# Kernel tuning notes

Measured on AMD Instinct MI355X. Metric: run time of the kernel, lower is better.

## Reference

```python
import jax, jax.numpy as jnp
import numpy as np

D_MODEL = 1024
N_HEADS = 16
HEAD_DIM = D_MODEL // N_HEADS
ROPE_THETA = 10000.0


def setup_inputs() -> dict:
    key = jax.random.key(0)
    ks = jax.random.split(key, 5)
    B, S = 4, 2048
    x = jax.random.normal(ks[0], (B, S, D_MODEL), dtype=jnp.float32)
    Wq = jax.random.normal(ks[1], (D_MODEL, D_MODEL), dtype=jnp.float32) * 0.02
    Wk = jax.random.normal(ks[2], (D_MODEL, D_MODEL), dtype=jnp.float32) * 0.02
    Wv = jax.random.normal(ks[3], (D_MODEL, D_MODEL), dtype=jnp.float32) * 0.02
    Wo = jax.random.normal(ks[4], (D_MODEL, D_MODEL), dtype=jnp.float32) * 0.02
    token_positions = jnp.arange(S, dtype=jnp.int32)
    return {"x": x, "token_positions": token_positions, "Wq": Wq, "Wk": Wk, "Wv": Wv, "Wo": Wo}


def apply_rope(t, positions):
    # t: [B, H, S, Dk]; positions: [S]
    half = HEAD_DIM // 2
    inv_freq = 1.0 / (ROPE_THETA ** (jnp.arange(half, dtype=jnp.float32) * 2.0 / HEAD_DIM))
    angles = positions.astype(jnp.float32)[:, None] * inv_freq[None, :]  # [S, half]
    cos = jnp.cos(angles)[None, None]  # [1,1,S,half]
    sin = jnp.sin(angles)[None, None]
    t_even = t[..., 0::2]
    t_odd = t[..., 1::2]
    rot_even = t_even * cos - t_odd * sin
    rot_odd = t_even * sin + t_odd * cos
    out = jnp.stack([rot_even, rot_odd], axis=-1)  # [B,H,S,half,2]
    return out.reshape(t.shape)


def reference(x, token_positions, Wq, Wk, Wv, Wo):
    B, S, _ = x.shape
    H, Dk = N_HEADS, HEAD_DIM
    # QKV projections, split heads -> [B, H, S, Dk]
    q = (x @ Wq).reshape(B, S, H, Dk).transpose(0, 2, 1, 3)
    k = (x @ Wk).reshape(B, S, H, Dk).transpose(0, 2, 1, 3)
    v = (x @ Wv).reshape(B, S, H, Dk).transpose(0, 2, 1, 3)
    q = apply_rope(q, token_positions)
    k = apply_rope(k, token_positions)
    scale = 1.0 / jnp.sqrt(jnp.asarray(Dk, dtype=x.dtype))
    scores = jnp.einsum('bhqd,bhkd->bhqk', q, k) * scale
    causal = jnp.tril(jnp.ones((S, S), dtype=bool))
    scores = jnp.where(causal[None, None], scores, jnp.asarray(-jnp.inf, dtype=scores.dtype))
    attn = jax.nn.softmax(scores, axis=-1)
    ctx = jnp.einsum('bhqk,bhkd->bhqd', attn, v)  # [B,H,S,Dk]
    ctx = ctx.transpose(0, 2, 1, 3).reshape(B, S, H * Dk)
    return ctx @ Wo
```

## Files before the change

kernel.cpp:

```cpp
#include <hip/hip_runtime.h>

typedef unsigned short u16;
typedef unsigned int   u32;
typedef __bf16  bf16x8 __attribute__((ext_vector_type(8)));
typedef float   f32x4  __attribute__((ext_vector_type(4)));
typedef float   f32x16 __attribute__((ext_vector_type(16)));
typedef u16     u16x4  __attribute__((ext_vector_type(4)));
typedef u16     u16x8  __attribute__((ext_vector_type(8)));
typedef u32     u32x4  __attribute__((ext_vector_type(4)));

#define D_MODEL 1024
#define N_HEADS 16
#define HEAD_DIM 64
#define BATCH 4
#define SEQ 2048
#define MROWS (BATCH*SEQ)

__device__ __forceinline__ u16 f2bf(float f){
  unsigned u = __builtin_bit_cast(unsigned, f);
  u += 0x7fffu + ((u >> 16) & 1u);
  return (u16)(u >> 16);
}
__device__ __forceinline__ float bf2f(u16 h){
  unsigned u = ((unsigned)h) << 16;
  return __builtin_bit_cast(float, u);
}
__device__ __forceinline__ u32 cvtpk(float a, float b){
  u32 r; asm("v_cvt_pk_bf16_f32 %0, %1, %2" : "=v"(r) : "v"(a), "v"(b)); return r;
}
__device__ __forceinline__ void gload_lds16(const u16* g, u16* l){
  __builtin_amdgcn_global_load_lds((const __attribute__((address_space(1))) void*)g,
                                   (__attribute__((address_space(3))) void*)l, 16, 0, 0);
}
#define MFMA16(a,b,c) __builtin_amdgcn_mfma_f32_16x16x32_bf16((a),(b),(c),0,0,0)

__global__ void k_prep(const float* __restrict__ x, const float* __restrict__ Wq,
                       const float* __restrict__ Wk, const float* __restrict__ Wv,
                       const float* __restrict__ Wo, const int* __restrict__ pos,
                       u16* __restrict__ xb, u16* __restrict__ wt, float2* __restrict__ tab){
  __shared__ float t[32][33];
  const int blk = blockIdx.x, tid = threadIdx.x;
  if (blk < 8192){
    int i = blk * 256 + tid;
    float4 v = reinterpret_cast<const float4*>(x)[i];
    u16x4 o;
    o.x = f2bf(v.x); o.y = f2bf(v.y); o.z = f2bf(v.z); o.w = f2bf(v.w);
    *reinterpret_cast<u16x4*>(xb + (size_t)i * 4) = o;
  } else if (blk < 12288){
    int idx = blk - 8192;
    int z = idx >> 10;
    int n0 = (idx & 31) * 32, k0 = ((idx >> 5) & 31) * 32;
    const float* W = (z==0)?Wq:(z==1)?Wk:(z==2)?Wv:Wo;
    u16* O = wt + (size_t)z * (D_MODEL*(size_t)D_MODEL);
    int tx = tid & 31, ty = tid >> 5;
    #pragma unroll
    for (int i = ty; i < 32; i += 8) t[i][tx] = W[(size_t)(k0+i)*D_MODEL + n0 + tx];
    __syncthreads();
    #pragma unroll
    for (int i = ty; i < 32; i += 8){
      int n = n0 + i;
      int np = n;
      if (z < 2){ int d = n & 63; np = (n & ~63) | ((d & 1) << 5) | (d >> 1); }
      O[(size_t)np*D_MODEL + k0 + tx] = f2bf(t[tx][i]);
    }
  } else {
    int i = (blk - 12288) * 256 + tid;
    int s = i >> 5, f = i & 31;
    float inv = exp2f(-(float)f * (13.287712379549449f / 32.0f));
    float a = (float)pos[s] * inv;
    float sn, cs;
    sincosf(a, &sn, &cs);
    tab[i] = make_float2(cs, sn);
  }
}

__global__ __launch_bounds__(512, 4) void k_gqkv(const u16* __restrict__ A, const u16* __restrict__ Bt,
                                                 const float2* __restrict__ tab,
                                                 u16* __restrict__ qout, u16* __restrict__ kout,
                                                 u16* __restrict__ vout){
  __shared__ u16 sh[3*12288];
  const int tid = threadIdx.x, lane = tid & 63, w = tid >> 6;
  const int lr = lane & 15, lg = lane >> 4;
  const int m0 = blockIdx.x * 128, n0 = blockIdx.y * 256;
  const int wm = w >> 2, wn = w & 3;
  const int ra = tid >> 2;
  const int sca = ((tid & 3) ^ ((ra >> 1) & 3)) << 3;
  const u16* gA  = A  + (size_t)(m0 + ra)*1024 + sca;
  const u16* gB0 = Bt + (size_t)(n0 + ra)*1024 + sca;
  const int rb1 = 128 + ra;
  const u16* gB1 = Bt + (size_t)(n0 + rb1)*1024 + (((tid & 3) ^ ((rb1 >> 1) & 3)) << 3);
  const int dA  = w*512;
  const int dB0 = 4096 + w*512;
  const int dB1 = 8192 + w*512;
  int aoff[4], boff[4];
  #pragma unroll
  for (int mi = 0; mi < 4; ++mi){ int r_ = wm*64 + mi*16 + lr; aoff[mi] = r_*32 + ((lg ^ ((r_>>1)&3)) << 3); }
  #pragma unroll
  for (int ni = 0; ni < 4; ++ni){ int r_ = wn*64 + ni*16 + lr; boff[ni] = 4096 + r_*32 + ((lg ^ ((r_>>1)&3)) << 3); }

  f32x4 acc[4][4] = {};
#define SA_(base, t)  gload_lds16(gA  + (size_t)(t)*32, sh + (base) + dA)
#define SB0_(base, t) gload_lds16(gB0 + (size_t)(t)*32, sh + (base) + dB0)
#define SB1_(base, t) gload_lds16(gB1 + (size_t)(t)*32, sh + (base) + dB1)
  SA_(0,0); SB0_(0,0); SB1_(0,0);
  SA_(12288,1); SB0_(12288,1); SB1_(12288,1);
  int b0 = 0, b1 = 12288, b2 = 24576;
  #pragma unroll 1
  for (int t = 0; t < 32; ++t){
    if (t < 31) { asm volatile("s_waitcnt vmcnt(3) lgkmcnt(0)" ::: "memory"); }
    else        { asm volatile("s_waitcnt vmcnt(0) lgkmcnt(0)" ::: "memory"); }
    __builtin_amdgcn_s_barrier();
    __builtin_amdgcn_sched_barrier(0);
    const u16* Sb = sh + b0;
    bf16x8 af0 = *(const bf16x8*)&Sb[aoff[0]];
    bf16x8 af1 = *(const bf16x8*)&Sb[aoff[1]];
    bf16x8 af2 = *(const bf16x8*)&Sb[aoff[2]];
    bf16x8 af3 = *(const bf16x8*)&Sb[aoff[3]];
    bf16x8 vb0 = *(const bf16x8*)&Sb[boff[0]];
    bf16x8 vb1 = *(const bf16x8*)&Sb[boff[1]];
    if (t < 30){ SA_(b2, t+2); }
    __builtin_amdgcn_s_setprio(1);
    acc[0][0] = MFMA16(af0, vb0, acc[0][0]);
    acc[1][0] = MFMA16(af1, vb0, acc[1][0]);
    acc[2][0] = MFMA16(af2, vb0, acc[2][0]);
    acc[3][0] = MFMA16(af3, vb0, acc[3][0]);
    acc[0][1] = MFMA16(af0, vb1, acc[0][1]);
    acc[1][1] = MFMA16(af1, vb1, acc[1][1]);
    acc[2][1] = MFMA16(af2, vb1, acc[2][1]);
    acc[3][1] = MFMA16(af3, vb1, acc[3][1]);
    __builtin_amdgcn_s_setprio(0);
    bf16x8 vb2 = *(const bf16x8*)&Sb[boff[2]];
    bf16x8 vb3 = *(const bf16x8*)&Sb[boff[3]];
    if (t < 30){ SB0_(b2, t+2); SB1_(b2, t+2); }
    __builtin_amdgcn_s_setprio(1);
    acc[0][2] = MFMA16(af0, vb2, acc[0][2]);
    acc[1][2] = MFMA16(af1, vb2, acc[1][2]);
    acc[2][2] = MFMA16(af2, vb2, acc[2][2]);
    acc[3][2] = MFMA16(af3, vb2, acc[3][2]);
    acc[0][3] = MFMA16(af0, vb3, acc[0][3]);
    acc[1][3] = MFMA16(af1, vb3, acc[1][3]);
    acc[2][3] = MFMA16(af2, vb3, acc[2][3]);
    acc[3][3] = MFMA16(af3, vb3, acc[3][3]);
    __builtin_amdgcn_s_setprio(0);
    int tmp = b0; b0 = b1; b1 = b2; b2 = tmp;
  }
#undef SA_
#undef SB0_
#undef SB1_

  const int which = n0 >> 10;
  #pragma unroll
  for (int mi = 0; mi < 4; mi++){
    int row = m0 + wm*64 + mi*16 + lg*4;
    #pragma unroll
    for (int ni = 0; ni < 4; ni++){
      int col = n0 + wn*64 + ni*16 + lr;
      int cm = col & 1023;
      int hh = cm >> 6, d = cm & 63;
      f32x4 vv = acc[mi][ni];
      f32x4 vp = acc[mi][ni ^ 2];
      #pragma unroll
      for (int r = 0; r < 4; r++){
        int rr = row + r;
        int bb = rr >> 11, s = rr & (SEQ-1);
        float val = vv[r];
        if (which < 2){
          float e = (ni < 2) ? val : vp[r];
          float o = (ni < 2) ? vp[r] : val;
          float2 cs = tab[s*32 + ((ni & 1) << 4) + lr];
          float ov = (ni < 2) ? (e*cs.x - o*cs.y) : (e*cs.y + o*cs.x);
          if (which == 0){
            ov *= 0.18033688011112042f;
            qout[(size_t)rr*1024 + cm] = f2bf(ov);
          } else {
            kout[(((size_t)(bb*N_HEADS + hh))*SEQ + s)*64 + d] = f2bf(ov);
          }
        } else {
          vout[(((size_t)(bb*N_HEADS + hh))*(SEQ/16) + (s >> 4))*1024 + d*16 + (s & 15)] = f2bf(val);
        }
      }
    }
  }
}

__global__ __launch_bounds__(256, 4) void k_gwo(const u16* __restrict__ A, const u16* __restrict__ Bt,
                                                float* __restrict__ fout){
  __shared__ u16 sh[3*8192];
  const int tid = threadIdx.x, lane = tid & 63, w = tid >> 6;
  const int lr = lane & 15, lg = lane >> 4;
  const int m0 = blockIdx.x * 128, n0 = blockIdx.y * 128;
  const int wm = w >> 1, wn = w & 1;
  const int ra = w*16 + (lane >> 2);
  const int sc = ((lane & 3) ^ ((ra >> 1) & 3)) << 3;
  const u16* gA0 = A  + (size_t)(m0 + ra)*1024 + sc;
  const u16* gA1 = A  + (size_t)(m0 + 64 + ra)*1024 + sc;
  const u16* gB0 = Bt + (size_t)(n0 + ra)*1024 + sc;
  const u16* gB1 = Bt + (size_t)(n0 + 64 + ra)*1024 + sc;
  int aoff[4], boff[4];
  #pragma unroll
  for (int mi = 0; mi < 4; ++mi){ int r_ = wm*64 + mi*16 + lr; aoff[mi] = r_*32 + ((lg ^ ((r_>>1)&3)) << 3); }
  #pragma unroll
  for (int ni = 0; ni < 4; ++ni){ int r_ = wn*64 + ni*16 + lr; boff[ni] = 4096 + r_*32 + ((lg ^ ((r_>>1)&3)) << 3); }
  f32x4 acc[4][4] = {};
#define SAW(base, t) { gload_lds16(gA0 + (size_t)(t)*32, sh + (base) + w*512); \
                       gload_lds16(gA1 + (size_t)(t)*32, sh + (base) + 2048 + w*512); }
#define SBW(base, t) { gload_lds16(gB0 + (size_t)(t)*32, sh + (base) + 4096 + w*512); \
                       gload_lds16(gB1 + (size_t)(t)*32, sh + (base) + 6144 + w*512); }
  SAW(0,0) SBW(0,0)
  SAW(8192,1) SBW(8192,1)
  int b0 = 0, b1 = 8192, b2 = 16384;
  #pragma unroll 1
  for (int t = 0; t < 32; ++t){
    if (t < 31) { asm volatile("s_waitcnt vmcnt(4) lgkmcnt(0)" ::: "memory"); }
    else        { asm volatile("s_waitcnt vmcnt(0) lgkmcnt(0)" ::: "memory"); }
    __builtin_amdgcn_s_barrier();
    __builtin_amdgcn_sched_barrier(0);
    const u16* Sb = sh + b0;
    bf16x8 af0 = *(const bf16x8*)&Sb[aoff[0]];
    bf16x8 af1 = *(const bf16x8*)&Sb[aoff[1]];
    bf16x8 af2 = *(const bf16x8*)&Sb[aoff[2]];
    bf16x8 af3 = *(const bf16x8*)&Sb[aoff[3]];
    bf16x8 vb0 = *(const bf16x8*)&Sb[boff[0]];
    bf16x8 vb1 = *(const bf16x8*)&Sb[boff[1]];
    if (t < 30){ SAW(b2, t+2) }
    __builtin_amdgcn_s_setprio(1);
    acc[0][0] = MFMA16(af0, vb0, acc[0][0]);
    acc[1][0] = MFMA16(af1, vb0, acc[1][0]);
    acc[2][0] = MFMA16(af2, vb0, acc[2][0]);
    acc[3][0] = MFMA16(af3, vb0, acc[3][0]);
    acc[0][1] = MFMA16(af0, vb1, acc[0][1]);
    acc[1][1] = MFMA16(af1, vb1, acc[1][1]);
    acc[2][1] = MFMA16(af2, vb1, acc[2][1]);
    acc[3][1] = MFMA16(af3, vb1, acc[3][1]);
    __builtin_amdgcn_s_setprio(0);
    bf16x8 vb2 = *(const bf16x8*)&Sb[boff[2]];
    bf16x8 vb3 = *(const bf16x8*)&Sb[boff[3]];
    if (t < 30){ SBW(b2, t+2) }
    __builtin_amdgcn_s_setprio(1);
    acc[0][2] = MFMA16(af0, vb2, acc[0][2]);
    acc[1][2] = MFMA16(af1, vb2, acc[1][2]);
    acc[2][2] = MFMA16(af2, vb2, acc[2][2]);
    acc[3][2] = MFMA16(af3, vb2, acc[3][2]);
    acc[0][3] = MFMA16(af0, vb3, acc[0][3]);
    acc[1][3] = MFMA16(af1, vb3, acc[1][3]);
    acc[2][3] = MFMA16(af2, vb3, acc[2][3]);
    acc[3][3] = MFMA16(af3, vb3, acc[3][3]);
    __builtin_amdgcn_s_setprio(0);
    int tmp = b0; b0 = b1; b1 = b2; b2 = tmp;
  }
#undef SAW
#undef SBW
  #pragma unroll
  for (int mi = 0; mi < 4; mi++){
    int row = m0 + wm*64 + mi*16 + lg*4;
    #pragma unroll
    for (int ni = 0; ni < 4; ni++){
      int col = n0 + wn*64 + ni*16 + lr;
      f32x4 vv = acc[mi][ni];
      #pragma unroll
      for (int r = 0; r < 4; r++)
        fout[(size_t)(row + r)*1024 + col] = vv[r];
    }
  }
}

__global__ __launch_bounds__(256, 3) void k_attn(const u16* __restrict__ q, const u16* __restrict__ k2,
                                                 const u16* __restrict__ v2, u16* __restrict__ ctx){
  __shared__ u16 kv[2][8192];
  const int lane = threadIdx.x & 63, w = threadIdx.x >> 6;
  const int lq = lane & 31, hl = lane >> 5;
  const int B = blockIdx.x;
  const int bh = B & 63, g = 15 - (B >> 6);
  const int b = bh >> 4, h = bh & 15;
  const int qi = 4*g + w;
  const int q0 = qi * 32;
  const int qmax0 = (4*g + 3) * 32;
  const u16* kglob = k2 + (size_t)bh*SEQ*64;
  const u16* vglob = v2 + (size_t)bh*(SEQ/16)*1024;

  const u16* qr_ = q + (size_t)(b*SEQ + q0 + lq)*D_MODEL + h*HEAD_DIM + hl*8;
  bf16x8 qf0 = *(const bf16x8*)&qr_[0];
  bf16x8 qf1 = *(const bf16x8*)&qr_[16];
  bf16x8 qf2 = *(const bf16x8*)&qr_[32];
  bf16x8 qf3 = *(const bf16x8*)&qr_[48];
  f32x16 acc0 = {}, acc1 = {};
  float m = -3.0e38f, l = 0.f;

  const int kr_ = (w<<3) + (lane>>3);
  const int kc_ = ((lane&7) ^ (lane>>3)) << 3;
  auto STAGE = [&](int bf, int jt){
    gload_lds16(kglob + (size_t)(jt      + kr_)*64 + kc_, &kv[bf][w<<9]);
    gload_lds16(kglob + (size_t)(jt + 32 + kr_)*64 + kc_, &kv[bf][2048 + (w<<9)]);
    gload_lds16(vglob + ((size_t)(jt>>4)<<10)        + (w<<9) + (lane<<3), &kv[bf][4096 + (w<<9)]);
    gload_lds16(vglob + ((size_t)((jt+32)>>4)<<10)   + (w<<9) + (lane<<3), &kv[bf][6144 + (w<<9)]);
  };

  STAGE(0, 0);
  __syncthreads();
  int p = 0;
  for (int j0 = 0; j0 <= qmax0; j0 += 64){
    if (j0 + 64 <= qmax0) STAGE(p^1, j0 + 64);
    if (j0 <= q0){
      const bool g2 = (j0 + 32 <= q0);
      const char* kb = (const char*)&kv[p][0];
      f32x16 S1 = {};
      {
        bf16x8 kf0 = *(const bf16x8*)(kb + lq*128 + (((0+hl) ^ (lq&7))<<4));
        bf16x8 kf1 = *(const bf16x8*)(kb + lq*128 + (((2+hl) ^ (lq&7))<<4));
        bf16x8 kf2 = *(const bf16x8*)(kb + lq*128 + (((4+hl) ^ (lq&7))<<4));
        bf16x8 kf3 = *(const bf16x8*)(kb + lq*128 + (((6+hl) ^ (lq&7))<<4));
        S1 = __builtin_amdgcn_mfma_f32_32x32x16_bf16(kf0, qf0, S1, 0, 0, 0);
        S1 = __builtin_amdgcn_mfma_f32_32x32x16_bf16(kf1, qf1, S1, 0, 0, 0);
        S1 = __builtin_amdgcn_mfma_f32_32x32x16_bf16(kf2, qf2, S1, 0, 0, 0);
        S1 = __builtin_amdgcn_mfma_f32_32x32x16_bf16(kf3, qf3, S1, 0, 0, 0);
      }
      if (j0 == q0){
        #pragma unroll
        for (int r = 0; r < 16; ++r){
          int kk = (r & 3) + 8*(r >> 2) + 4*hl;
          if (kk > lq) S1[r] = -3.0e38f;
        }
      }
      f32x16 S2 = {};
      if (g2){
        const char* kb2 = kb + 4096;
        bf16x8 kf0 = *(const bf16x8*)(kb2 + lq*128 + (((0+hl) ^ (lq&7))<<4));
        bf16x8 kf1 = *(const bf16x8*)(kb2 + lq*128 + (((2+hl) ^ (lq&7))<<4));
        bf16x8 kf2 = *(const bf16x8*)(kb2 + lq*128 + (((4+hl) ^ (lq&7))<<4));
        bf16x8 kf3 = *(const bf16x8*)(kb2 + lq*128 + (((6+hl) ^ (lq&7))<<4));
        S2 = __builtin_amdgcn_mfma_f32_32x32x16_bf16(kf0, qf0, S2, 0, 0, 0);
        S2 = __builtin_amdgcn_mfma_f32_32x32x16_bf16(kf1, qf1, S2, 0, 0, 0);
        S2 = __builtin_amdgcn_mfma_f32_32x32x16_bf16(kf2, qf2, S2, 0, 0, 0);
        S2 = __builtin_amdgcn_mfma_f32_32x32x16_bf16(kf3, qf3, S2, 0, 0, 0);
        if (j0 + 32 == q0){
          #pragma unroll
          for (int r = 0; r < 16; ++r){
            int kk = (r & 3) + 8*(r >> 2) + 4*hl;
            if (kk > lq) S2[r] = -3.0e38f;
          }
        }
      }
      float pm = fmaxf(fmaxf(fmaxf(S1[0],S1[1]), fmaxf(S1[2],S1[3])),
                       fmaxf(fmaxf(S1[4],S1[5]), fmaxf(S1[6],S1[7])));
      pm = fmaxf(pm, fmaxf(fmaxf(fmaxf(S1[8],S1[9]), fmaxf(S1[10],S1[11])),
                           fmaxf(fmaxf(S1[12],S1[13]),fmaxf(S1[14],S1[15]))));
      if (g2){
        float pm2 = fmaxf(fmaxf(fmaxf(S2[0],S2[1]), fmaxf(S2[2],S2[3])),
                          fmaxf(fmaxf(S2[4],S2[5]), fmaxf(S2[6],S2[7])));
        pm2 = fmaxf(pm2, fmaxf(fmaxf(fmaxf(S2[8],S2[9]), fmaxf(S2[10],S2[11])),
                               fmaxf(fmaxf(S2[12],S2[13]),fmaxf(S2[14],S2[15]))));
        pm = fmaxf(pm, pm2);
      }
      pm = fmaxf(pm, __shfl_xor(pm, 32));
      if (__any(pm > m + 8.f)){
        float mn = fmaxf(m, pm);
        float cr = __builtin_amdgcn_exp2f(m - mn);
        l *= cr;
        #pragma unroll
        for (int r = 0; r < 16; ++r){ acc0[r] *= cr; acc1[r] *= cr; }
        m = mn;
      }
      #pragma unroll
      for (int r = 0; r < 16; ++r) S1[r] = __builtin_amdgcn_exp2f(S1[r] - m);
      l += ((S1[0]+S1[1])+(S1[2]+S1[3])) + ((S1[4]+S1[5])+(S1[6]+S1[7]))
         + ((S1[8]+S1[9])+(S1[10]+S1[11])) + ((S1[12]+S1[13])+(S1[14]+S1[15]));
      {
        u32 g0a = cvtpk(S1[0], S1[1]),  g0b = cvtpk(S1[2], S1[3]);
        u32 g1a = cvtpk(S1[4], S1[5]),  g1b = cvtpk(S1[6], S1[7]);
        u32 g2a = cvtpk(S1[8], S1[9]),  g2b = cvtpk(S1[10],S1[11]);
        u32 g3a = cvtpk(S1[12],S1[13]), g3b = cvtpk(S1[14],S1[15]);
        u32 s0a = hl ? g0a : g1a, s0b = hl ? g0b : g1b;
        u32 e0a = (u32)__shfl_xor((int)s0a, 32), e0b = (u32)__shfl_xor((int)s0b, 32);
        u32 m0a = hl ? g1a : g0a, m0b = hl ? g1b : g0b;
        u32 s1a = hl ? g2a : g3a, s1b = hl ? g2b : g3b;
        u32 e1a = (u32)__shfl_xor((int)s1a, 32), e1b = (u32)__shfl_xor((int)s1b, 32);
        u32 m1a = hl ? g3a : g2a, m1b = hl ? g3b : g2b;
        u32x4 A0 = { hl ? e0a : m0a, hl ? e0b : m0b, hl ? m0a : e0a, hl ? m0b : e0b };
        u32x4 A1 = { hl ? e1a : m1a, hl ? e1b : m1b, hl ? m1a : e1a, hl ? m1b : e1b };
        bf16x8 pa0 = __builtin_bit_cast(bf16x8, A0);
        bf16x8 pa1 = __builtin_bit_cast(bf16x8, A1);
        const char* vb = kb + 8192;
        bf16x8 vf00 = *(const bf16x8*)(vb + lq*32 + hl*16);
        bf16x8 vf01 = *(const bf16x8*)(vb + lq*32 + hl*16 + 1024);
        bf16x8 vf10 = *(const bf16x8*)(vb + lq*32 + hl*16 + 2048);
        bf16x8 vf11 = *(const bf16x8*)(vb + lq*32 + hl*16 + 3072);
        acc0 = __builtin_amdgcn_mfma_f32_32x32x16_bf16(vf00, pa0, acc0, 0, 0, 0);
        acc0 = __builtin_amdgcn_mfma_f32_32x32x16_bf16(vf10, pa1, acc0, 0, 0, 0);
        acc1 = __builtin_amdgcn_mfma_f32_32x32x16_bf16(vf01, pa0, acc1, 0, 0, 0);
        acc1 = __builtin_amdgcn_mfma_f32_32x32x16_bf16(vf11, pa1, acc1, 0, 0, 0);
      }
      if (g2){
        #pragma unroll
        for (int r = 0; r < 16; ++r) S2[r] = __builtin_amdgcn_exp2f(S2[r] - m);
        l += ((S2[0]+S2[1])+(S2[2]+S2[3])) + ((S2[4]+S2[5])+(S2[6]+S2[7]))
           + ((S2[8]+S2[9])+(S2[10]+S2[11])) + ((S2[12]+S2[13])+(S2[14]+S2[15]));
        u32 g0a = cvtpk(S2[0], S2[1]),  g0b = cvtpk(S2[2], S2[3]);
        u32 g1a = cvtpk(S2[4], S2[5]),  g1b = cvtpk(S2[6], S2[7]);
        u32 g2a_ = cvtpk(S2[8], S2[9]), g2b_ = cvtpk(S2[10],S2[11]);
        u32 g3a = cvtpk(S2[12],S2[13]), g3b = cvtpk(S2[14],S2[15]);
        u32 s0a = hl ? g0a : g1a, s0b = hl ? g0b : g1b;
        u32 e0a = (u32)__shfl_xor((int)s0a, 32), e0b = (u32)__shfl_xor((int)s0b, 32);
        u32 m0a = hl ? g1a : g0a, m0b = hl ? g1b : g0b;
        u32 s1a = hl ? g2a_ : g3a, s1b = hl ? g2b_ : g3b;
        u32 e1a = (u32)__shfl_xor((int)s1a, 32), e1b = (u32)__shfl_xor((int)s1b, 32);
        u32 m1a = hl ? g3a : g2a_, m1b = hl ? g3b : g2b_;
        u32x4 A0 = { hl ? e0a : m0a, hl ? e0b : m0b, hl ? m0a : e0a, hl ? m0b : e0b };
        u32x4 A1 = { hl ? e1a : m1a, hl ? e1b : m1b, hl ? m1a : e1a, hl ? m1b : e1b };
        bf16x8 pa0 = __builtin_bit_cast(bf16x8, A0);
        bf16x8 pa1 = __builtin_bit_cast(bf16x8, A1);
        const char* vb = kb + 12288;
        bf16x8 vf00 = *(const bf16x8*)(vb + lq*32 + hl*16);
        bf16x8 vf01 = *(const bf16x8*)(vb + lq*32 + hl*16 + 1024);
        bf16x8 vf10 = *(const bf16x8*)(vb + lq*32 + hl*16 + 2048);
        bf16x8 vf11 = *(const bf16x8*)(vb + lq*32 + hl*16 + 3072);
        acc0 = __builtin_amdgcn_mfma_f32_32x32x16_bf16(vf00, pa0, acc0, 0, 0, 0);
        acc0 = __builtin_amdgcn_mfma_f32_32x32x16_bf16(vf10, pa1, acc0, 0, 0, 0);
        acc1 = __builtin_amdgcn_mfma_f32_32x32x16_bf16(vf01, pa0, acc1, 0, 0, 0);
        acc1 = __builtin_amdgcn_mfma_f32_32x32x16_bf16(vf11, pa1, acc1, 0, 0, 0);
      }
    }
    __syncthreads();
    p ^= 1;
  }
  l += __shfl_xor(l, 32);
  float inv = __builtin_amdgcn_rcpf(l);
  char* tbc = (char*)kv + w*4096;
  #pragma unroll
  for (int r = 0; r < 16; ++r){
    int d0 = (r & 3) + 8*(r >> 2) + 4*hl;
    *(u16*)(tbc + lq*128 + ((2*d0)      ^ ((lq & 7) << 4))) = f2bf(acc0[r] * inv);
    *(u16*)(tbc + lq*128 + ((2*(d0+32)) ^ ((lq & 7) << 4))) = f2bf(acc1[r] * inv);
  }
  int qr2 = lane >> 1, chb = (lane & 1) * 4;
  u16* cp = ctx + (size_t)(b*SEQ + q0 + qr2)*D_MODEL + h*HEAD_DIM;
  #pragma unroll
  for (int i = 0; i < 4; ++i){
    int ch = chb + i;
    u16x8 vv = *(const u16x8*)(tbc + qr2*128 + 16*(ch ^ (qr2 & 7)));
    *(u16x8*)&cp[ch*8] = vv;
  }
}

extern "C" void kernel_launch(void* const* d_in, const int* in_sizes, int n_in,
                              void* d_out, int out_size, void* d_ws, size_t ws_size,
                              hipStream_t stream){
  const float* x  = (const float*)d_in[0];
  const int*  pos = (const int*)d_in[1];
  const float* Wq = (const float*)d_in[2];
  const float* Wk = (const float*)d_in[3];
  const float* Wv = (const float*)d_in[4];
  const float* Wo = (const float*)d_in[5];
  float* out = (float*)d_out;
  char* ws = (char*)d_ws;
  u16* xb   = (u16*)(ws);
  u16* wt   = (u16*)(ws + 16777216);
  u16* qb   = (u16*)(ws + 25165824);
  u16* kbh  = (u16*)(ws + 41943040);
  u16* vt2  = (u16*)(ws + 58720256);
  float2* tab = (float2*)(ws + 75497472);
  u16* ctxb = xb;

  k_prep<<<12544, 256, 0, stream>>>(x, Wq, Wk, Wv, Wo, pos, xb, wt, tab);
  k_gqkv<<<dim3(64,12), 512, 0, stream>>>(xb, wt, tab, qb, kbh, vt2);
  k_attn<<<dim3(1024), 256, 0, stream>>>(qb, kbh, vt2, ctxb);
  k_gwo<<<dim3(64,8), 256, 0, stream>>>(ctxb, wt + 3145728, out);
}
```

Before: 176.4 us.

## Widen output-projection GEMM tile to 128x256 with 512-thread blocks

After: 174.8 us. About the same (-0.9%).

```diff
diff --git a/kernel.cpp b/kernel.cpp
--- a/kernel.cpp
+++ b/kernel.cpp
@@ -183,35 +183,38 @@
   }
 }
 
-__global__ __launch_bounds__(256, 4) void k_gwo(const u16* __restrict__ A, const u16* __restrict__ Bt,
-                                                float* __restrict__ fout){
-  __shared__ u16 sh[3*8192];
+__global__ __launch_bounds__(512, 4) void k_gwo2(const u16* __restrict__ A, const u16* __restrict__ Bt,
+                                                 float* __restrict__ fout){
+  __shared__ u16 sh[3*12288];
   const int tid = threadIdx.x, lane = tid & 63, w = tid >> 6;
   const int lr = lane & 15, lg = lane >> 4;
-  const int m0 = blockIdx.x * 128, n0 = blockIdx.y * 128;
-  const int wm = w >> 1, wn = w & 1;
-  const int ra = w*16 + (lane >> 2);
-  const int sc = ((lane & 3) ^ ((ra >> 1) & 3)) << 3;
-  const u16* gA0 = A  + (size_t)(m0 + ra)*1024 + sc;
-  const u16* gA1 = A  + (size_t)(m0 + 64 + ra)*1024 + sc;
-  const u16* gB0 = Bt + (size_t)(n0 + ra)*1024 + sc;
-  const u16* gB1 = Bt + (size_t)(n0 + 64 + ra)*1024 + sc;
+  const int m0 = blockIdx.x * 128, n0 = blockIdx.y * 256;
+  const int wm = w >> 2, wn = w & 3;
+  const int ra = tid >> 2;
+  const int sca = ((tid & 3) ^ ((ra >> 1) & 3)) << 3;
+  const u16* gA  = A  + (size_t)(m0 + ra)*1024 + sca;
+  const u16* gB0 = Bt + (size_t)(n0 + ra)*1024 + sca;
+  const int rb1 = 128 + ra;
+  const u16* gB1 = Bt + (size_t)(n0 + rb1)*1024 + (((tid & 3) ^ ((rb1 >> 1) & 3)) << 3);
+  const int dA  = w*512;
+  const int dB0 = 4096 + w*512;
+  const int dB1 = 8192 + w*512;
   int aoff[4], boff[4];
   #pragma unroll
   for (int mi = 0; mi < 4; ++mi){ int r_ = wm*64 + mi*16 + lr; aoff[mi] = r_*32 + ((lg ^ ((r_>>1)&3)) << 3); }
   #pragma unroll
   for (int ni = 0; ni < 4; ++ni){ int r_ = wn*64 + ni*16 + lr; boff[ni] = 4096 + r_*32 + ((lg ^ ((r_>>1)&3)) << 3); }
+
   f32x4 acc[4][4] = {};
-#define SAW(base, t) { gload_lds16(gA0 + (size_t)(t)*32, sh + (base) + w*512); \
-                       gload_lds16(gA1 + (size_t)(t)*32, sh + (base) + 2048 + w*512); }
-#define SBW(base, t) { gload_lds16(gB0 + (size_t)(t)*32, sh + (base) + 4096 + w*512); \
-                       gload_lds16(gB1 + (size_t)(t)*32, sh + (base) + 6144 + w*512); }
-  SAW(0,0) SBW(0,0)
-  SAW(8192,1) SBW(8192,1)
-  int b0 = 0, b1 = 8192, b2 = 16384;
+#define SA_(base, t)  gload_lds16(gA  + (size_t)(t)*32, sh + (base) + dA)
+#define SB0_(base, t) gload_lds16(gB0 + (size_t)(t)*32, sh + (base) + dB0)
+#define SB1_(base, t) gload_lds16(gB1 + (size_t)(t)*32, sh + (base) + dB1)
+  SA_(0,0); SB0_(0,0); SB1_(0,0);
+  SA_(12288,1); SB0_(12288,1); SB1_(12288,1);
+  int b0 = 0, b1 = 12288, b2 = 24576;
   #pragma unroll 1
   for (int t = 0; t < 32; ++t){
-    if (t < 31) { asm volatile("s_waitcnt vmcnt(4) lgkmcnt(0)" ::: "memory"); }
+    if (t < 31) { asm volatile("s_waitcnt vmcnt(3) lgkmcnt(0)" ::: "memory"); }
     else        { asm volatile("s_waitcnt vmcnt(0) lgkmcnt(0)" ::: "memory"); }
     __builtin_amdgcn_s_barrier();
     __builtin_amdgcn_sched_barrier(0);
@@ -222,7 +225,7 @@
     bf16x8 af3 = *(const bf16x8*)&Sb[aoff[3]];
     bf16x8 vb0 = *(const bf16x8*)&Sb[boff[0]];
     bf16x8 vb1 = *(const bf16x8*)&Sb[boff[1]];
-    if (t < 30){ SAW(b2, t+2) }
+    if (t < 30){ SA_(b2, t+2); }
     __builtin_amdgcn_s_setprio(1);
     acc[0][0] = MFMA16(af0, vb0, acc[0][0]);
     acc[1][0] = MFMA16(af1, vb0, acc[1][0]);
@@ -235,7 +238,7 @@
     __builtin_amdgcn_s_setprio(0);
     bf16x8 vb2 = *(const bf16x8*)&Sb[boff[2]];
     bf16x8 vb3 = *(const bf16x8*)&Sb[boff[3]];
-    if (t < 30){ SBW(b2, t+2) }
+    if (t < 30){ SB0_(b2, t+2); SB1_(b2, t+2); }
     __builtin_amdgcn_s_setprio(1);
     acc[0][2] = MFMA16(af0, vb2, acc[0][2]);
     acc[1][2] = MFMA16(af1, vb2, acc[1][2]);
@@ -248,8 +251,10 @@
     __builtin_amdgcn_s_setprio(0);
     int tmp = b0; b0 = b1; b1 = b2; b2 = tmp;
   }
-#undef SAW
-#undef SBW
+#undef SA_
+#undef SB0_
+#undef SB1_
+
   #pragma unroll
   for (int mi = 0; mi < 4; mi++){
     int row = m0 + wm*64 + mi*16 + lg*4;
@@ -463,5 +468,5 @@
   k_prep<<<12544, 256, 0, stream>>>(x, Wq, Wk, Wv, Wo, pos, xb, wt, tab);
   k_gqkv<<<dim3(64,12), 512, 0, stream>>>(xb, wt, tab, qb, kbh, vt2);
   k_attn<<<dim3(1024), 256, 0, stream>>>(qb, kbh, vt2, ctxb);
-  k_gwo<<<dim3(64,8), 256, 0, stream>>>(ctxb, wt + 3145728, out);
-}
+  k_gwo2<<<dim3(64,4), 512, 0, stream>>>(ctxb, wt + 3145728, out);
+}
```
